# Kernel tuning notes

Hardware: AMD Instinct MI355X
Metric: run time of the kernel (lower is better)

The kernel has to match this reference:

```python
import jax, jax.numpy as jnp
import numpy as np

EPS = 1e-5

def _linear(x, w, b):
    # torch nn.Linear convention: w is [out, in]
    return jnp.einsum('...i,oi->...o', x, w) + b

def _l2_normalize(x, axis=-1):
    n = jnp.sqrt(jnp.sum(x * x, axis=axis, keepdims=True))
    return x / jnp.maximum(n, 1e-12)

def _online_softmax_scan(sim):
    # sim: [B, H, L]. Running max m_t and running sum s_t = sum_{i<=t} exp(sim_i - m_t)
    def combine(a, b):
        ma, sa = a
        mb, sb = b
        m = jnp.maximum(ma, mb)
        s = sa * jnp.exp(ma - m) + sb * jnp.exp(mb - m)
        return m, s
    m_scan, s_scan = jax.lax.associative_scan(combine, (sim, jnp.ones_like(sim)), axis=2)
    return m_scan, s_scan


def setup_inputs() -> dict:
    key = jax.random.key(0)
    ks = jax.random.split(key, 8)
    B, L, D = 2, 2048, 256
    H, h = 8, 32
    s = 1.0 / np.sqrt(D)
    inp = {
        'x': jax.random.normal(ks[0], (B, L, D), jnp.float32),
        'wq_w': jax.random.normal(ks[1], (D, D), jnp.float32) * s,
        'wq_b': jnp.zeros((D,), jnp.float32),
        'wk_w': jax.random.normal(ks[2], (D, D), jnp.float32) * s,
        'wk_b': jnp.zeros((D,), jnp.float32),
        'wv_w': jax.random.normal(ks[3], (D, D), jnp.float32) * s,
        'wv_b': jnp.zeros((D,), jnp.float32),
        'wo_w': jax.random.normal(ks[4], (D, D), jnp.float32) * s,
        'wo_b': jnp.zeros((D,), jnp.float32),
        'wg_w': jax.random.normal(ks[5], (1, h * h), jnp.float32) * (1.0 / np.sqrt(h * h)),
        'wg_b': jnp.zeros((1,), jnp.float32),
        'kv_norm_scale': jnp.ones((1, H, 1, h, h), jnp.float32),
        'qk_norm_scale': jnp.full((1, H, 1), 1.0 / np.sqrt(h), jnp.float32),
    }
    return inp


def reference(x, wq_w, wq_b, wk_w, wk_b, wv_w, wv_b, wo_w, wo_b,
              wg_w, wg_b, kv_norm_scale, qk_norm_scale):
    B, L, D = x.shape
    H, h = kv_norm_scale.shape[1], kv_norm_scale.shape[3]

    q = _linear(x, wq_w, wq_b).reshape(B, L, H, h).transpose(0, 2, 1, 3)  # bhld
    k = _linear(x, wk_w, wk_b).reshape(B, L, H, h).transpose(0, 2, 1, 3)
    v = _linear(x, wv_w, wv_b).reshape(B, L, H, h).transpose(0, 2, 1, 3)

    sim = jnp.einsum('bhld,bhld->bhl', q, k) * qk_norm_scale  # [B,H,L]

    k = _l2_normalize(k)
    v = _l2_normalize(v)

    # outer-product KV state per position: [B,H,L,h,h]
    Z = jnp.einsum('bhld,bhle->bhlde', v, k) * kv_norm_scale

    # gating: squared ReLU of linear over flattened h*h features
    gate_inputs = Z.reshape(B, H, L, h * h)
    gates_logits = jnp.einsum('bhli,oi->bhlo', gate_inputs, wg_w) + wg_b  # [B,H,L,1]
    gates = jnp.square(jax.nn.relu(gates_logits)) + EPS
    gates = gates[..., None]  # [B,H,L,1,1]
    gated_Z = gates * Z

    # associative scans along L
    m_scan, s_scan = _online_softmax_scan(sim)        # [B,H,L]
    Z_scan = jnp.cumsum(gated_Z, axis=2)              # [B,H,L,h,h]
    g_scan = jnp.cumsum(gates, axis=2)                # [B,H,L,1,1]

    softmax_weights = (jnp.exp(sim - m_scan) / (s_scan + EPS))[..., None, None]
    gated_weights = Z_scan / (g_scan + EPS)
    attn_weights = gated_weights * (1.0 + jax.nn.silu(softmax_weights))

    ctxt = jnp.einsum('bhld,bhlde->bhle', q, attn_weights)
    ctxt = ctxt.transpose(0, 2, 1, 3).reshape(B, L, D)
    return _linear(ctxt, wo_w, wo_b)
```

## Files before the change

### kernel.cpp

```cpp
#include <hip/hip_runtime.h>
#include <math.h>

#define EPSV 1e-5f

static constexpr int Ls = 2048, Hh = 8;
static constexpr int NCH = 64, T = 32;

__global__ __launch_bounds__(256) void gemm_kernel(
    const float* __restrict__ A,
    const float* __restrict__ w0, const float* __restrict__ b0,
    const float* __restrict__ w1, const float* __restrict__ b1,
    const float* __restrict__ w2, const float* __restrict__ b2,
    float* __restrict__ o0, float* __restrict__ o1, float* __restrict__ o2,
    int mode)
{
    constexpr int LDT = 68;
    __shared__ float As[16 * LDT];
    __shared__ float Ws[16 * LDT];
    const int tid = threadIdx.x;
    const int mt = blockIdx.x, nt = blockIdx.y;

    const float *Wp, *bp;
    float* Op;
    int ncol0;
    if (mode == 0) {
        const int which = nt >> 2;
        ncol0 = (nt & 3) * 64;
        Wp = which == 0 ? w0 : (which == 1 ? w1 : w2);
        bp = which == 0 ? b0 : (which == 1 ? b1 : b2);
        Op = which == 0 ? o0 : (which == 1 ? o1 : o2);
    } else {
        ncol0 = nt * 64;
        Wp = w0; bp = b0; Op = o0;
    }

    const int tx = tid & 15, ty = tid >> 4;
    const int m0 = mt * 64;
    const int lrow = tid >> 2, lc4 = (tid & 3) * 4;
    float acc[4][4] = {};

    for (int k0 = 0; k0 < 256; k0 += 16) {
        const float4 av = *(const float4*)&A[(size_t)(m0 + lrow) * 256 + k0 + lc4];
        const float4 wv = *(const float4*)&Wp[(size_t)(ncol0 + lrow) * 256 + k0 + lc4];
        As[(lc4 + 0) * LDT + lrow] = av.x;
        As[(lc4 + 1) * LDT + lrow] = av.y;
        As[(lc4 + 2) * LDT + lrow] = av.z;
        As[(lc4 + 3) * LDT + lrow] = av.w;
        Ws[(lc4 + 0) * LDT + lrow] = wv.x;
        Ws[(lc4 + 1) * LDT + lrow] = wv.y;
        Ws[(lc4 + 2) * LDT + lrow] = wv.z;
        Ws[(lc4 + 3) * LDT + lrow] = wv.w;
        __syncthreads();
#pragma unroll
        for (int kk = 0; kk < 16; ++kk) {
            const float4 a4 = *(const float4*)&As[kk * LDT + ty * 4];
            const float4 w4 = *(const float4*)&Ws[kk * LDT + tx * 4];
            const float a[4] = {a4.x, a4.y, a4.z, a4.w};
            const float w[4] = {w4.x, w4.y, w4.z, w4.w};
#pragma unroll
            for (int i = 0; i < 4; ++i)
#pragma unroll
                for (int j = 0; j < 4; ++j)
                    acc[i][j] = fmaf(a[i], w[j], acc[i][j]);
        }
        __syncthreads();
    }

    float bias[4];
#pragma unroll
    for (int j = 0; j < 4; ++j) bias[j] = bp[ncol0 + tx * 4 + j];

    if (mode == 0) {
#pragma unroll
        for (int i = 0; i < 4; ++i) {
            const int rm = m0 + ty * 4 + i;
            const int b = rm >> 11, l = rm & (Ls - 1);
#pragma unroll
            for (int j = 0; j < 4; ++j) {
                const int o = ncol0 + tx * 4 + j;
                const int hd = o >> 5, e = o & 31;
                Op[(((size_t)(b * Hh + hd)) * Ls + l) * 32 + e] = acc[i][j] + bias[j];
            }
        }
    } else {
#pragma unroll
        for (int i = 0; i < 4; ++i) {
            const int rm = m0 + ty * 4 + i;
#pragma unroll
            for (int j = 0; j < 4; ++j)
                Op[(size_t)rm * 256 + ncol0 + tx * 4 + j] = acc[i][j] + bias[j];
        }
    }
}

__global__ __launch_bounds__(1024) void chunk_sum_kernel(
    const float* __restrict__ qh, float* __restrict__ kh, float* __restrict__ vh,
    const float* __restrict__ wg_w, const float* __restrict__ wg_b,
    const float* __restrict__ kvs, const float* __restrict__ qks,
    float* __restrict__ simG, float* __restrict__ gG,
    float* __restrict__ ZcT, float* __restrict__ mT, float* __restrict__ sT,
    float* __restrict__ gTt)
{
    __shared__ float lkn[1024], lvn[1024], lwk[1024], lsim[T], lg[T];
    const int tid = threadIdx.x;
    const int c = blockIdx.x, bh = blockIdx.y, h = bh & 7;
    const int l = tid >> 5, lane = tid & 31;
    const size_t base = ((size_t)bh * Ls + c * T) * 32;

    const float qv = qh[base + tid];
    const float kv = kh[base + tid];
    const float vv = vh[base + tid];
    lwk[tid] = wg_w[tid] * kvs[h * 1024 + tid];

    float qk = qv * kv, ks = kv * kv, vs = vv * vv;
#pragma unroll
    for (int off = 16; off; off >>= 1) {
        qk += __shfl_xor(qk, off);
        ks += __shfl_xor(ks, off);
        vs += __shfl_xor(vs, off);
    }
    const float kn = kv / fmaxf(sqrtf(ks), 1e-12f);
    const float vn = vv / fmaxf(sqrtf(vs), 1e-12f);
    kh[base + tid] = kn;
    vh[base + tid] = vn;
    lkn[tid] = kn;
    lvn[tid] = vn;
    if (lane == 0) {
        const float s = qk * qks[h];
        lsim[l] = s;
        simG[bh * Ls + c * T + l] = s;
    }
    __syncthreads();

    float t = 0.f;
#pragma unroll 8
    for (int d = 0; d < 32; ++d)
        t = fmaf(lvn[l * 32 + d], lwk[d * 32 + lane], t);
    t *= lkn[l * 32 + lane];
#pragma unroll
    for (int off = 16; off; off >>= 1) t += __shfl_xor(t, off);
    if (lane == 0) {
        const float r = fmaxf(t + wg_b[0], 0.f);
        const float g = r * r + EPSV;
        lg[l] = g;
        gG[bh * Ls + c * T + l] = g;
    }
    __syncthreads();

    {
        const int e = tid & 31, d = tid >> 5;
        float z = 0.f;
#pragma unroll 8
        for (int l2 = 0; l2 < T; ++l2)
            z = fmaf(lg[l2] * lvn[l2 * 32 + d], lkn[l2 * 32 + e], z);
        ZcT[((size_t)bh * NCH + c) * 1024 + tid] = z;
    }

    if (tid < 32) {
        float m = lsim[tid], s = 1.f, g = lg[tid];
#pragma unroll
        for (int off = 16; off; off >>= 1) {
            const float mo = __shfl_xor(m, off);
            const float so = __shfl_xor(s, off);
            const float mn = fmaxf(m, mo);
            s = s * __expf(m - mn) + so * __expf(mo - mn);
            m = mn;
            g += __shfl_xor(g, off);
        }
        if (tid == 0) {
            mT[bh * NCH + c] = m;
            sT[bh * NCH + c] = s;
            gTt[bh * NCH + c] = g;
        }
    }
}

__global__ __launch_bounds__(256) void prefix_kernel(
    float* __restrict__ Zc, float* __restrict__ mT, float* __restrict__ sT,
    float* __restrict__ gTt,
    const float* __restrict__ kvs, float* __restrict__ aW, float* __restrict__ bW,
    int* __restrict__ flagW)
{
    const int bh = blockIdx.x, seg = blockIdx.y;
    const int tid = threadIdx.x;
    const int el = seg * 256 + tid;
    float* Zb = Zc + (size_t)bh * NCH * 1024 + el;

    float run = 0.f;
#pragma unroll
    for (int cb = 0; cb < NCH; cb += 8) {
        float v[8];
#pragma unroll
        for (int i = 0; i < 8; ++i) v[i] = Zb[(size_t)(cb + i) * 1024];
#pragma unroll
        for (int i = 0; i < 8; ++i) {
            const float t = v[i];
            Zb[(size_t)(cb + i) * 1024] = run;
            run += t;
        }
    }

    if (seg == 0 && tid < 64) {
        float m = mT[bh * NCH + tid], s = sT[bh * NCH + tid], g = gTt[bh * NCH + tid];
#pragma unroll
        for (int off = 1; off < 64; off <<= 1) {
            const float mo = __shfl_up(m, off);
            const float so = __shfl_up(s, off);
            const float go = __shfl_up(g, off);
            if (tid >= off) {
                const float mn = fmaxf(m, mo);
                s = s * __expf(m - mn) + so * __expf(mo - mn);
                m = mn;
                g += go;
            }
        }
        float me = __shfl_up(m, 1), se = __shfl_up(s, 1), ge = __shfl_up(g, 1);
        if (tid == 0) { me = -1e30f; se = 0.f; ge = 0.f; }
        mT[bh * NCH + tid] = me;
        sT[bh * NCH + tid] = se;
        gTt[bh * NCH + tid] = ge;
    }

    if (bh == 0 && seg == 3) {
        const int h = tid >> 5, e = tid & 31;
        const float* K = kvs + h * 1024;
        const float k00 = K[0];
        int ok = (k00 != 0.0f);
        for (int d = 0; d < 32; ++d) {
            const float lhs = K[d * 32 + e] * k00;
            const float rhs = K[d * 32] * K[e];
            const float diff = fabsf(lhs - rhs);
            if (diff > 1e-6f * fmaxf(fmaxf(fabsf(lhs), fabsf(rhs)), 1e-20f)) ok = 0;
        }
        aW[h * 32 + e] = K[e * 32];
        bW[h * 32 + e] = (k00 != 0.0f) ? K[e] / k00 : 0.f;
        const int allok = __syncthreads_and(ok);
        if (tid == 0) flagW[0] = allok;
    }
}

__global__ __launch_bounds__(1024) void chunk_out_kernel(
    const float* __restrict__ qh, const float* __restrict__ knG, const float* __restrict__ vnG,
    const float* __restrict__ simG, const float* __restrict__ gG,
    const float* __restrict__ kvs,
    const float* __restrict__ ZcP, const float* __restrict__ mP,
    const float* __restrict__ sP, const float* __restrict__ gP,
    const float* __restrict__ aW, const float* __restrict__ bW,
    const int* __restrict__ flagW,
    float* __restrict__ ctxt)
{
    __shared__ float qa[1024], knb[1024], zp[1024], lkvs[1024];
    __shared__ float vnT[32 * 33], sW[32 * 33];
    __shared__ float la[32], lb[32], lg[T], lsim[T], lwgt[T];
    const int tid = threadIdx.x;
    const int c = blockIdx.x, bh = blockIdx.y, h = bh & 7, b = bh >> 3;
    const int l = tid >> 5, lane = tid & 31;
    const size_t base = ((size_t)bh * Ls + c * T) * 32;
    const int flag = flagW[0];

    const float qv = qh[base + tid];
    const float knv = knG[base + tid];
    const float vnv = vnG[base + tid];
    vnT[lane * 33 + l] = vnv;
    zp[tid] = ZcP[((size_t)bh * NCH + c) * 1024 + tid];
    if (!flag) lkvs[tid] = kvs[h * 1024 + tid];
    if (tid < 32) {
        la[tid] = aW[h * 32 + tid];
        lb[tid] = bW[h * 32 + tid];
        lg[tid] = gG[bh * Ls + c * T + tid];
        lsim[tid] = simG[bh * Ls + c * T + tid];
    }
    __syncthreads();

    qa[tid] = flag ? qv * la[lane] : qv;
    knb[tid] = flag ? knv * lb[lane] : knv;
    if (tid < 32) {
        float m = lsim[tid], s = 1.f, g = lg[tid];
#pragma unroll
        for (int off = 1; off < 32; off <<= 1) {
            const float mo = __shfl_up(m, off);
            const float so = __shfl_up(s, off);
            const float go = __shfl_up(g, off);
            if (tid >= off) {
                const float mn = fmaxf(m, mo);
                s = s * __expf(m - mn) + so * __expf(mo - mn);
                m = mn;
                g += go;
            }
        }
        const float mp = mP[bh * NCH + c];
        const float sp = sP[bh * NCH + c];
        const float gp = gP[bh * NCH + c];
        const float mn = fmaxf(mp, m);
        s = sp * __expf(mp - mn) + s * __expf(m - mn);
        m = mn;
        g += gp;
        const float sw = __expf(lsim[tid] - m) / (s + EPSV);
        const float sig = 1.f / (1.f + __expf(-sw));
        lwgt[tid] = (1.f + sw * sig) / (g + EPSV);
    }
    __syncthreads();

    if (flag) {
        float s = 0.f, y0 = 0.f;
        const float4* qa4 = (const float4*)&qa[l * 32];
#pragma unroll
        for (int d4 = 0; d4 < 8; ++d4) {
            const float4 q4 = qa4[d4];
            const int d = d4 * 4;
            s = fmaf(q4.x, vnT[(d + 0) * 33 + lane], s);
            s = fmaf(q4.y, vnT[(d + 1) * 33 + lane], s);
            s = fmaf(q4.z, vnT[(d + 2) * 33 + lane], s);
            s = fmaf(q4.w, vnT[(d + 3) * 33 + lane], s);
            y0 = fmaf(q4.x, zp[(d + 0) * 32 + lane], y0);
            y0 = fmaf(q4.y, zp[(d + 1) * 32 + lane], y0);
            y0 = fmaf(q4.z, zp[(d + 2) * 32 + lane], y0);
            y0 = fmaf(q4.w, zp[(d + 3) * 32 + lane], y0);
        }
        sW[l * 33 + lane] = (lane <= l) ? lg[lane] * s : 0.f;
        __syncthreads();
        float y = y0 * lb[lane];
#pragma unroll 8
        for (int j = 0; j < 32; ++j)
            y = fmaf(sW[l * 33 + j], knb[j * 32 + lane], y);
        y *= lwgt[l];
        ctxt[((size_t)(b * Ls + c * T + l)) * 256 + h * 32 + lane] = y;
    } else {
        float qe[32];
#pragma unroll
        for (int d = 0; d < 32; ++d)
            qe[d] = qa[l * 32 + d] * lkvs[d * 32 + lane];
        float y = 0.f;
#pragma unroll
        for (int d = 0; d < 32; ++d)
            y = fmaf(qe[d], zp[d * 32 + lane], y);
        for (int j = 0; j < 32; ++j) {
            float s = 0.f;
#pragma unroll
            for (int d = 0; d < 32; ++d)
                s = fmaf(qe[d], vnT[d * 33 + j], s);
            if (j <= l) y = fmaf(lg[j] * s, knb[j * 32 + lane], y);
        }
        y *= lwgt[l];
        ctxt[((size_t)(b * Ls + c * T + l)) * 256 + h * 32 + lane] = y;
    }
}

extern "C" void kernel_launch(void* const* d_in, const int* in_sizes, int n_in,
                              void* d_out, int out_size, void* d_ws, size_t ws_size,
                              hipStream_t stream) {
    const float* x    = (const float*)d_in[0];
    const float* wq_w = (const float*)d_in[1];
    const float* wq_b = (const float*)d_in[2];
    const float* wk_w = (const float*)d_in[3];
    const float* wk_b = (const float*)d_in[4];
    const float* wv_w = (const float*)d_in[5];
    const float* wv_b = (const float*)d_in[6];
    const float* wo_w = (const float*)d_in[7];
    const float* wo_b = (const float*)d_in[8];
    const float* wg_w = (const float*)d_in[9];
    const float* wg_b = (const float*)d_in[10];
    const float* kvs  = (const float*)d_in[11];
    const float* qks  = (const float*)d_in[12];
    float* out = (float*)d_out;

    float* ws = (float*)d_ws;
    float* qh   = out;
    float* kh   = ws;
    float* vh   = kh + 1048576;
    float* simG = vh + 1048576;
    float* gG   = simG + 32768;
    float* ZcT  = gG + 32768;
    float* mT   = ZcT + 1048576;
    float* sT   = mT + 1024;
    float* gTt  = sT + 1024;
    float* aW   = gTt + 1024;
    float* bW   = aW + 256;
    int*   flagW = (int*)(bW + 256);
    float* ctxt = bW + 256 + 4;

    gemm_kernel<<<dim3(64, 12), 256, 0, stream>>>(
        x, wq_w, wq_b, wk_w, wk_b, wv_w, wv_b, qh, kh, vh, 0);
    chunk_sum_kernel<<<dim3(NCH, 16), 1024, 0, stream>>>(
        qh, kh, vh, wg_w, wg_b, kvs, qks, simG, gG, ZcT, mT, sT, gTt);
    prefix_kernel<<<dim3(16, 4), 256, 0, stream>>>(
        ZcT, mT, sT, gTt, kvs, aW, bW, flagW);
    chunk_out_kernel<<<dim3(NCH, 16), 1024, 0, stream>>>(
        qh, kh, vh, simG, gG, kvs, ZcT, mT, sT, gTt, aW, bW, flagW, ctxt);
    gemm_kernel<<<dim3(64, 4), 256, 0, stream>>>(
        ctxt, wo_w, wo_b, nullptr, nullptr, nullptr, nullptr, out, nullptr, nullptr, 1);
}
```

Before: 161.9 us.

## Replace FP32 SIMT GEMMs with split-bf16 MFMA GEMMs for projections

Replaces the scalar FP32 tiled GEMM for the QKV and output projections with an MFMA kernel. Each FP32 operand is split into bf16 hi/lo parts and three MFMA products (hi*hi, hi*lo, lo*hi) are accumulated to approximate FP32 accuracy. A new convert kernel pre-splits x and the weights every call, and chunk_out now writes ctxt directly as hi/lo bf16. This adds an extra launch plus extra memory traffic for the split arrays, and some precision loss from dropping the lo*lo term.

```diff
diff --git a/kernel.cpp b/kernel.cpp
--- a/kernel.cpp
+++ b/kernel.cpp
@@ -6,90 +6,146 @@
 static constexpr int Ls = 2048, Hh = 8;
 static constexpr int NCH = 64, T = 32;
 
-__global__ __launch_bounds__(256) void gemm_kernel(
-    const float* __restrict__ A,
-    const float* __restrict__ w0, const float* __restrict__ b0,
-    const float* __restrict__ w1, const float* __restrict__ b1,
-    const float* __restrict__ w2, const float* __restrict__ b2,
-    float* __restrict__ o0, float* __restrict__ o1, float* __restrict__ o2,
+typedef unsigned short u16;
+using frag  = __attribute__((ext_vector_type(8))) short;
+using f32x4 = __attribute__((ext_vector_type(4))) float;
+
+__device__ __forceinline__ void split_bf16(float v, u16& hi, u16& lo) {
+    const unsigned u = __float_as_uint(v);
+    hi = (u16)(u >> 16);
+    const float hf = __uint_as_float((unsigned)hi << 16);
+    lo = (u16)(__float_as_uint(v - hf) >> 16);
+}
+
+__global__ __launch_bounds__(256) void convert_kernel(
+    const float* __restrict__ x, const float* __restrict__ wq,
+    const float* __restrict__ wk, const float* __restrict__ wv,
+    const float* __restrict__ wo,
+    u16* __restrict__ xhi, u16* __restrict__ xlo,
+    u16* __restrict__ whi, u16* __restrict__ wlo)
+{
+    const int gi = blockIdx.x * 256 + threadIdx.x;
+    const float* src;
+    u16 *dhi, *dlo;
+    size_t off;
+    if (gi < 262144) {
+        src = x; off = gi; dhi = xhi; dlo = xlo;
+    } else {
+        const int t = gi - 262144;
+        const int w = t >> 14, o = t & 16383;
+        src = w == 0 ? wq : w == 1 ? wk : w == 2 ? wv : wo;
+        off = o;
+        dhi = whi + (size_t)w * 65536;
+        dlo = wlo + (size_t)w * 65536;
+    }
+    const float4 v = ((const float4*)src)[off];
+    ushort4 h, l;
+    split_bf16(v.x, h.x, l.x);
+    split_bf16(v.y, h.y, l.y);
+    split_bf16(v.z, h.z, l.z);
+    split_bf16(v.w, h.w, l.w);
+    ((ushort4*)dhi)[off] = h;
+    ((ushort4*)dlo)[off] = l;
+}
+
+__global__ __launch_bounds__(256) void mfma_gemm(
+    const u16* __restrict__ Ahi, const u16* __restrict__ Alo,
+    const u16* __restrict__ Whi_all, const u16* __restrict__ Wlo_all,
+    const float* __restrict__ bq, const float* __restrict__ bk, const float* __restrict__ bv,
+    float* __restrict__ oq, float* __restrict__ ok_, float* __restrict__ ov,
     int mode)
 {
-    constexpr int LDT = 68;
-    __shared__ float As[16 * LDT];
-    __shared__ float Ws[16 * LDT];
+    constexpr int LDK = 40;
+    __shared__ u16 As_hi[128 * LDK], As_lo[128 * LDK];
+    __shared__ u16 Bs_hi[64 * LDK],  Bs_lo[64 * LDK];
+
     const int tid = threadIdx.x;
     const int mt = blockIdx.x, nt = blockIdx.y;
-
-    const float *Wp, *bp;
+    int ncol0, which;
+    const float* bp;
     float* Op;
-    int ncol0;
     if (mode == 0) {
-        const int which = nt >> 2;
+        which = nt >> 2;
         ncol0 = (nt & 3) * 64;
-        Wp = which == 0 ? w0 : (which == 1 ? w1 : w2);
-        bp = which == 0 ? b0 : (which == 1 ? b1 : b2);
-        Op = which == 0 ? o0 : (which == 1 ? o1 : o2);
+        bp = which == 0 ? bq : which == 1 ? bk : bv;
+        Op = which == 0 ? oq : which == 1 ? ok_ : ov;
     } else {
+        which = 3;
         ncol0 = nt * 64;
-        Wp = w0; bp = b0; Op = o0;
-    }
-
-    const int tx = tid & 15, ty = tid >> 4;
-    const int m0 = mt * 64;
-    const int lrow = tid >> 2, lc4 = (tid & 3) * 4;
-    float acc[4][4] = {};
-
-    for (int k0 = 0; k0 < 256; k0 += 16) {
-        const float4 av = *(const float4*)&A[(size_t)(m0 + lrow) * 256 + k0 + lc4];
-        const float4 wv = *(const float4*)&Wp[(size_t)(ncol0 + lrow) * 256 + k0 + lc4];
-        As[(lc4 + 0) * LDT + lrow] = av.x;
-        As[(lc4 + 1) * LDT + lrow] = av.y;
-        As[(lc4 + 2) * LDT + lrow] = av.z;
-        As[(lc4 + 3) * LDT + lrow] = av.w;
-        Ws[(lc4 + 0) * LDT + lrow] = wv.x;
-        Ws[(lc4 + 1) * LDT + lrow] = wv.y;
-        Ws[(lc4 + 2) * LDT + lrow] = wv.z;
-        Ws[(lc4 + 3) * LDT + lrow] = wv.w;
+        bp = bq;
+        Op = oq;
+    }
+    const u16* Whi = Whi_all + (size_t)which * 65536;
+    const u16* Wlo = Wlo_all + (size_t)which * 65536;
+
+    const int m0 = mt * 128;
+    const int srow = tid >> 2, skc = tid & 3;
+    const int wave = tid >> 6, lane = tid & 63;
+    const int l15 = lane & 15, quad = lane >> 4;
+    const int wm0 = (wave >> 1) * 64, wn0 = (wave & 1) * 32;
+
+    f32x4 acc[4][2] = {};
+
+    for (int k0 = 0; k0 < 256; k0 += 32) {
+        const size_t ga0 = (size_t)(m0 + srow) * 256 + k0 + skc * 8;
+        const size_t ga1 = (size_t)(m0 + 64 + srow) * 256 + k0 + skc * 8;
+        const size_t gb  = (size_t)(ncol0 + srow) * 256 + k0 + skc * 8;
+        const uint4 ah0 = *(const uint4*)&Ahi[ga0];
+        const uint4 ah1 = *(const uint4*)&Ahi[ga1];
+        const uint4 al0 = *(const uint4*)&Alo[ga0];
+        const uint4 al1 = *(const uint4*)&Alo[ga1];
+        const uint4 bh0 = *(const uint4*)&Whi[gb];
+        const uint4 bl0 = *(const uint4*)&Wlo[gb];
         __syncthreads();
-#pragma unroll
-        for (int kk = 0; kk < 16; ++kk) {
-            const float4 a4 = *(const float4*)&As[kk * LDT + ty * 4];
-            const float4 w4 = *(const float4*)&Ws[kk * LDT + tx * 4];
-            const float a[4] = {a4.x, a4.y, a4.z, a4.w};
-            const float w[4] = {w4.x, w4.y, w4.z, w4.w};
-#pragma unroll
-            for (int i = 0; i < 4; ++i)
-#pragma unroll
-                for (int j = 0; j < 4; ++j)
-                    acc[i][j] = fmaf(a[i], w[j], acc[i][j]);
-        }
+        *(uint4*)&As_hi[srow * LDK + skc * 8] = ah0;
+        *(uint4*)&As_hi[(64 + srow) * LDK + skc * 8] = ah1;
+        *(uint4*)&As_lo[srow * LDK + skc * 8] = al0;
+        *(uint4*)&As_lo[(64 + srow) * LDK + skc * 8] = al1;
+        *(uint4*)&Bs_hi[srow * LDK + skc * 8] = bh0;
+        *(uint4*)&Bs_lo[srow * LDK + skc * 8] = bl0;
         __syncthreads();
-    }
-
-    float bias[4];
-#pragma unroll
-    for (int j = 0; j < 4; ++j) bias[j] = bp[ncol0 + tx * 4 + j];
-
-    if (mode == 0) {
-#pragma unroll
-        for (int i = 0; i < 4; ++i) {
-            const int rm = m0 + ty * 4 + i;
-            const int b = rm >> 11, l = rm & (Ls - 1);
-#pragma unroll
-            for (int j = 0; j < 4; ++j) {
-                const int o = ncol0 + tx * 4 + j;
-                const int hd = o >> 5, e = o & 31;
-                Op[(((size_t)(b * Hh + hd)) * Ls + l) * 32 + e] = acc[i][j] + bias[j];
+
+        frag ah[4], al[4], bh[2], bl[2];
+#pragma unroll
+        for (int tm = 0; tm < 4; ++tm) {
+            const int r = wm0 + tm * 16 + l15;
+            ah[tm] = *(const frag*)&As_hi[r * LDK + quad * 8];
+            al[tm] = *(const frag*)&As_lo[r * LDK + quad * 8];
+        }
+#pragma unroll
+        for (int tn = 0; tn < 2; ++tn) {
+            const int r = wn0 + tn * 16 + l15;
+            bh[tn] = *(const frag*)&Bs_hi[r * LDK + quad * 8];
+            bl[tn] = *(const frag*)&Bs_lo[r * LDK + quad * 8];
+        }
+#pragma unroll
+        for (int tm = 0; tm < 4; ++tm)
+#pragma unroll
+            for (int tn = 0; tn < 2; ++tn) {
+                acc[tm][tn] = __builtin_amdgcn_mfma_f32_16x16x32_bf16(ah[tm], bh[tn], acc[tm][tn], 0, 0, 0);
+                acc[tm][tn] = __builtin_amdgcn_mfma_f32_16x16x32_bf16(ah[tm], bl[tn], acc[tm][tn], 0, 0, 0);
+                acc[tm][tn] = __builtin_amdgcn_mfma_f32_16x16x32_bf16(al[tm], bh[tn], acc[tm][tn], 0, 0, 0);
             }
-        }
-    } else {
-#pragma unroll
-        for (int i = 0; i < 4; ++i) {
-            const int rm = m0 + ty * 4 + i;
-#pragma unroll
-            for (int j = 0; j < 4; ++j)
-                Op[(size_t)rm * 256 + ncol0 + tx * 4 + j] = acc[i][j] + bias[j];
-        }
+    }
+
+#pragma unroll
+    for (int tn = 0; tn < 2; ++tn) {
+        const int o = ncol0 + wn0 + tn * 16 + l15;
+        const float bias = bp[o];
+        const int hd = o >> 5, e = o & 31;
+#pragma unroll
+        for (int tm = 0; tm < 4; ++tm)
+#pragma unroll
+            for (int r = 0; r < 4; ++r) {
+                const int rm = m0 + wm0 + tm * 16 + quad * 4 + r;
+                const float val = acc[tm][tn][r] + bias;
+                if (mode == 0) {
+                    const int b = rm >> 11, l = rm & (Ls - 1);
+                    Op[(((size_t)(b * Hh + hd)) * Ls + l) * 32 + e] = val;
+                } else {
+                    Op[(size_t)rm * 256 + o] = val;
+                }
+            }
     }
 }
 
@@ -247,7 +303,7 @@
     const float* __restrict__ sP, const float* __restrict__ gP,
     const float* __restrict__ aW, const float* __restrict__ bW,
     const int* __restrict__ flagW,
-    float* __restrict__ ctxt)
+    u16* __restrict__ chi, u16* __restrict__ clo)
 {
     __shared__ float qa[1024], knb[1024], zp[1024], lkvs[1024];
     __shared__ float vnT[32 * 33], sW[32 * 33];
@@ -301,6 +357,7 @@
     }
     __syncthreads();
 
+    float y;
     if (flag) {
         float s = 0.f, y0 = 0.f;
         const float4* qa4 = (const float4*)&qa[l * 32];
@@ -319,18 +376,17 @@
         }
         sW[l * 33 + lane] = (lane <= l) ? lg[lane] * s : 0.f;
         __syncthreads();
-        float y = y0 * lb[lane];
+        y = y0 * lb[lane];
 #pragma unroll 8
         for (int j = 0; j < 32; ++j)
             y = fmaf(sW[l * 33 + j], knb[j * 32 + lane], y);
         y *= lwgt[l];
-        ctxt[((size_t)(b * Ls + c * T + l)) * 256 + h * 32 + lane] = y;
     } else {
         float qe[32];
 #pragma unroll
         for (int d = 0; d < 32; ++d)
             qe[d] = qa[l * 32 + d] * lkvs[d * 32 + lane];
-        float y = 0.f;
+        y = 0.f;
 #pragma unroll
         for (int d = 0; d < 32; ++d)
             y = fmaf(qe[d], zp[d * 32 + lane], y);
@@ -342,8 +398,12 @@
             if (j <= l) y = fmaf(lg[j] * s, knb[j * 32 + lane], y);
         }
         y *= lwgt[l];
-        ctxt[((size_t)(b * Ls + c * T + l)) * 256 + h * 32 + lane] = y;
-    }
+    }
+    u16 hi, lo;
+    split_bf16(y, hi, lo);
+    const size_t oidx = ((size_t)(b * Ls + c * T + l)) * 256 + h * 32 + lane;
+    chi[oidx] = hi;
+    clo[oidx] = lo;
 }
 
 extern "C" void kernel_launch(void* const* d_in, const int* in_sizes, int n_in,
@@ -364,29 +424,35 @@
     const float* qks  = (const float*)d_in[12];
     float* out = (float*)d_out;
 
-    float* ws = (float*)d_ws;
-    float* qh   = out;
-    float* kh   = ws;
+    u16* xhi = (u16*)d_ws;
+    u16* xlo = xhi + 1048576;
+    u16* whi = xlo + 1048576;
+    u16* wlo = whi + 262144;
+    u16* chi = wlo + 262144;
+    u16* clo = chi + 1048576;
+    float* qh   = (float*)(clo + 1048576);
+    float* kh   = qh + 1048576;
     float* vh   = kh + 1048576;
-    float* simG = vh + 1048576;
+    float* ZcT  = vh + 1048576;
+    float* simG = ZcT + 1048576;
     float* gG   = simG + 32768;
-    float* ZcT  = gG + 32768;
-    float* mT   = ZcT + 1048576;
+    float* mT   = gG + 32768;
     float* sT   = mT + 1024;
     float* gTt  = sT + 1024;
     float* aW   = gTt + 1024;
     float* bW   = aW + 256;
-    int*   flagW = (int*)(bW + 256);
-    float* ctxt = bW + 256 + 4;
-
-    gemm_kernel<<<dim3(64, 12), 256, 0, stream>>>(
-        x, wq_w, wq_b, wk_w, wk_b, wv_w, wv_b, qh, kh, vh, 0);
+    int* flagW  = (int*)(bW + 256);
+
+    convert_kernel<<<1280, 256, 0, stream>>>(
+        x, wq_w, wk_w, wv_w, wo_w, xhi, xlo, whi, wlo);
+    mfma_gemm<<<dim3(32, 12), 256, 0, stream>>>(
+        xhi, xlo, whi, wlo, wq_b, wk_b, wv_b, qh, kh, vh, 0);
     chunk_sum_kernel<<<dim3(NCH, 16), 1024, 0, stream>>>(
         qh, kh, vh, wg_w, wg_b, kvs, qks, simG, gG, ZcT, mT, sT, gTt);
     prefix_kernel<<<dim3(16, 4), 256, 0, stream>>>(
         ZcT, mT, sT, gTt, kvs, aW, bW, flagW);
     chunk_out_kernel<<<dim3(NCH, 16), 1024, 0, stream>>>(
-        qh, kh, vh, simG, gG, kvs, ZcT, mT, sT, gTt, aW, bW, flagW, ctxt);
-    gemm_kernel<<<dim3(64, 4), 256, 0, stream>>>(
-        ctxt, wo_w, wo_b, nullptr, nullptr, nullptr, nullptr, out, nullptr, nullptr, 1);
-}
+        qh, kh, vh, simG, gG, kvs, ZcT, mT, sT, gTt, aW, bW, flagW, chi, clo);
+    mfma_gemm<<<dim3(32, 4), 256, 0, stream>>>(
+        chi, clo, whi, wlo, wo_b, nullptr, nullptr, out, nullptr, nullptr, 1);
+}
```

Measured after the change: 147.3 us. 1.1x faster.
